# Kernel optimization log

Hardware: AMD Instinct MI355X
Metric: run time of the kernel (lower is better)

The kernel has to match this reference:

```python
import jax, jax.numpy as jnp
import numpy as np

B, T, C = 4, 2048, 1024
N_HEAD = 16
HEAD = C // N_HEAD

def setup_inputs() -> dict:
    key = jax.random.key(0)
    k1, k2, k3 = jax.random.split(key, 3)
    x = jax.random.normal(k1, (B, T, C), dtype=jnp.float32)
    w_attn = jax.random.normal(k2, (C, 3 * C), dtype=jnp.float32) * (1.0 / np.sqrt(C))
    w_proj = jax.random.normal(k3, (C, C), dtype=jnp.float32) * (1.0 / np.sqrt(C))
    return {"x": x, "w_attn": w_attn, "w_proj": w_proj}

def reference(x, w_attn, w_proj):
    b, t, c = x.shape
    qkv = x @ w_attn  # [B,T,3C]
    q, k, v = jnp.split(qkv, 3, axis=-1)
    # [B,T,C] -> [B,H,T,D]
    def heads(z):
        return z.reshape(b, t, N_HEAD, HEAD).transpose(0, 2, 1, 3)
    q, k, v = heads(q), heads(k), heads(v)
    scale = 1.0 / np.sqrt(HEAD)
    att = jnp.einsum('bhqd,bhkd->bhqk', q, k) * scale  # [B,H,T,T]
    causal = jnp.tril(jnp.ones((t, t), dtype=bool))
    att = jnp.where(causal[None, None], att, -jnp.inf)
    att = jax.nn.softmax(att, axis=-1)
    y = jnp.einsum('bhqk,bhkd->bhqd', att, v)  # [B,H,T,D]
    y = y.transpose(0, 2, 1, 3).reshape(b, t, c)
    return y @ w_proj
```

## Files before the change

kernel.cpp:

```cpp
#include <hip/hip_runtime.h>
#include <hip/hip_bf16.h>


typedef __attribute__((ext_vector_type(8))) short bf16x8;
typedef __attribute__((ext_vector_type(4))) float f32x4;
typedef __attribute__((ext_vector_type(16))) float f32x16;

#define T_DIM 2048
#define NHEAD 16
#define HDIM  64

__device__ __forceinline__ unsigned short f2bf(float f) {
    union { float f; unsigned int u; } v; v.f = f;
    unsigned int r = v.u + 0x7fffu + ((v.u >> 16) & 1u);
    return (unsigned short)(r >> 16);
}

__device__ __forceinline__ unsigned cvtpk_bf16(float lo, float hi) {
    unsigned r;
    asm("v_cvt_pk_bf16_f32 %0, %1, %2" : "=v"(r) : "v"(lo), "v"(hi));
    return r;
}
__device__ __forceinline__ void pl32swap(unsigned &x, unsigned &y) {
    asm("v_permlane32_swap_b32 %0, %1" : "+v"(x), "+v"(y));
}
__device__ __forceinline__ bf16x8 mk8(unsigned w0, unsigned w1, unsigned w2, unsigned w3) {
    union { unsigned u[4]; bf16x8 v; } p;
    p.u[0] = w0; p.u[1] = w1; p.u[2] = w2; p.u[3] = w3;
    return p.v;
}

__device__ __forceinline__ void gload_lds16(const void* g, void* l) {
    __builtin_amdgcn_global_load_lds(
        (const __attribute__((address_space(1))) void*)g,
        (__attribute__((address_space(3))) void*)l,
        16, 0, 0);
}

__global__ void cvt_bf16_k(const float* __restrict__ src, unsigned short* __restrict__ dst, int n) {
    int i = (blockIdx.x * blockDim.x + threadIdx.x) * 4;
    if (i < n) {
        float4 v = *(const float4*)(src + i);
        ushort4 o; o.x = f2bf(v.x); o.y = f2bf(v.y); o.z = f2bf(v.z); o.w = f2bf(v.w);
        *(ushort4*)(dst + i) = o;
    }
}

__global__ void transpose_wb_k(const float* __restrict__ src, unsigned short* __restrict__ dst,
                               int R, int Cc) {
    __shared__ float tile[32][33];
    int c0 = blockIdx.x * 32, r0 = blockIdx.y * 32;
    int tx = threadIdx.x & 31, ty = threadIdx.x >> 5;
    #pragma unroll
    for (int i = 0; i < 32; i += 8)
        tile[ty + i][tx] = src[(size_t)(r0 + ty + i) * Cc + c0 + tx];
    __syncthreads();
    #pragma unroll
    for (int i = 0; i < 32; i += 8)
        dst[(size_t)(c0 + ty + i) * R + r0 + tx] = f2bf(tile[tx][ty + i]);
}

template<int EPI>
__global__ __launch_bounds__(512, 2) void gemm_bt_k(
    const unsigned short* __restrict__ A, const unsigned short* __restrict__ Bt,
    void* __restrict__ out0, void* __restrict__ out1, void* __restrict__ out2,
    int M, int N, int K)
{
    extern __shared__ __align__(16) unsigned short smem[];
    unsigned short* sA = smem;
    unsigned short* sB = smem + 49152;

    const int tid = threadIdx.x, lane = tid & 63, wave = tid >> 6;
    const int wm = wave >> 1, wn = wave & 1;
    const int lrow = lane & 15, hi = lane >> 4;

    const int nwg = gridDim.x * gridDim.y;
    const int lin = blockIdx.y * gridDim.x + blockIdx.x;
    const int lin2 = (lin & 7) * (nwg >> 3) + (lin >> 3);
    const int bxg = lin2 % gridDim.x, byg = lin2 / gridDim.x;
    const int row0 = byg * 256, col0 = bxg * 128;

    const int arow = tid >> 3;
    const int gk = ((tid & 7) ^ (arow & 7)) * 8;
    const unsigned short* gA0 = A + (size_t)(row0 + arow) * K + gk;
    const unsigned short* gA1 = A + (size_t)(row0 + arow + 64) * K + gk;
    const unsigned short* gA2 = A + (size_t)(row0 + arow + 128) * K + gk;
    const unsigned short* gA3 = A + (size_t)(row0 + arow + 192) * K + gk;
    const unsigned short* gB0 = Bt + (size_t)(col0 + arow) * K + gk;
    const unsigned short* gB1 = Bt + (size_t)(col0 + arow + 64) * K + gk;

    const int NT = K >> 6;

#define STAGE_P0(ts, sl) { const size_t ko_ = (size_t)(ts) * 64; \
        unsigned short* dA_ = sA + (sl) * 16384; \
        gload_lds16(gA0 + ko_, dA_ + tid * 8); \
        gload_lds16(gA1 + ko_, dA_ + (tid + 512) * 8); \
        gload_lds16(gA2 + ko_, dA_ + (tid + 1024) * 8); }
#define STAGE_P1(ts, sl) { const size_t ko_ = (size_t)(ts) * 64; \
        unsigned short* dA_ = sA + (sl) * 16384; \
        unsigned short* dB_ = sB + (sl) * 8192; \
        gload_lds16(gA3 + ko_, dA_ + (tid + 1536) * 8); \
        gload_lds16(gB0 + ko_, dB_ + tid * 8); \
        gload_lds16(gB1 + ko_, dB_ + (tid + 512) * 8); }

    f32x4 acc[4][4] = {};

    STAGE_P0(0, 0); STAGE_P1(0, 0);
    STAGE_P0(1, 1); STAGE_P1(1, 1);
    asm volatile("s_waitcnt vmcnt(6)" ::: "memory");
    __builtin_amdgcn_s_barrier();
    __builtin_amdgcn_sched_barrier(0);

    int slot = 0;
    for (int t = 0; t < NT; ++t) {
        const int s2 = (slot + 2 >= 3) ? slot - 1 : slot + 2;
        const unsigned short* As = sA + slot * 16384;
        const unsigned short* Bs = sB + slot * 8192;
        bf16x8 af[4], bf_[4];

        {
            const int kc = hi ^ (lrow & 7);
            #pragma unroll
            for (int mi = 0; mi < 4; ++mi)
                af[mi] = *(const bf16x8*)&As[((wm * 64 + mi * 16 + lrow) * 8 + kc) * 8];
            #pragma unroll
            for (int ni = 0; ni < 4; ++ni)
                bf_[ni] = *(const bf16x8*)&Bs[((wn * 64 + ni * 16 + lrow) * 8 + kc) * 8];
        }
        if (t + 2 < NT) STAGE_P0(t + 2, s2);
        __builtin_amdgcn_s_barrier();
        asm volatile("s_waitcnt lgkmcnt(0)" ::: "memory");
        __builtin_amdgcn_sched_barrier(0);
        __builtin_amdgcn_s_setprio(1);
        #pragma unroll
        for (int mi = 0; mi < 4; ++mi)
            #pragma unroll
            for (int ni = 0; ni < 4; ++ni)
                acc[mi][ni] = __builtin_amdgcn_mfma_f32_16x16x32_bf16(af[mi], bf_[ni], acc[mi][ni], 0, 0, 0);
        __builtin_amdgcn_s_setprio(0);
        __builtin_amdgcn_s_barrier();

        {
            const int kc = (4 + hi) ^ (lrow & 7);
            #pragma unroll
            for (int mi = 0; mi < 4; ++mi)
                af[mi] = *(const bf16x8*)&As[((wm * 64 + mi * 16 + lrow) * 8 + kc) * 8];
            #pragma unroll
            for (int ni = 0; ni < 4; ++ni)
                bf_[ni] = *(const bf16x8*)&Bs[((wn * 64 + ni * 16 + lrow) * 8 + kc) * 8];
        }
        if (t + 2 < NT) STAGE_P1(t + 2, s2);
        __builtin_amdgcn_s_barrier();
        asm volatile("s_waitcnt lgkmcnt(0)" ::: "memory");
        __builtin_amdgcn_sched_barrier(0);
        __builtin_amdgcn_s_setprio(1);
        #pragma unroll
        for (int mi = 0; mi < 4; ++mi)
            #pragma unroll
            for (int ni = 0; ni < 4; ++ni)
                acc[mi][ni] = __builtin_amdgcn_mfma_f32_16x16x32_bf16(af[mi], bf_[ni], acc[mi][ni], 0, 0, 0);
        __builtin_amdgcn_s_setprio(0);
        if (t + 2 < NT) { asm volatile("s_waitcnt vmcnt(6)" ::: "memory"); }
        else           { asm volatile("s_waitcnt vmcnt(0)" ::: "memory"); }
        __builtin_amdgcn_s_barrier();
        __builtin_amdgcn_sched_barrier(0);
        slot = (slot + 1 >= 3) ? 0 : slot + 1;
    }
#undef STAGE_P0
#undef STAGE_P1

    if (EPI == 1) {
        #pragma unroll
        for (int mi = 0; mi < 4; ++mi)
            #pragma unroll
            for (int ni = 0; ni < 4; ++ni) {
                int gm0 = row0 + wm * 64 + mi * 16 + hi * 4;
                int gn  = col0 + wn * 64 + ni * 16 + lrow;
                #pragma unroll
                for (int r = 0; r < 4; ++r)
                    ((float*)out0)[(size_t)(gm0 + r) * N + gn] = acc[mi][ni][r];
            }
    } else if (col0 < 1024) {
        const int bb = row0 >> 11;
        #pragma unroll
        for (int mi = 0; mi < 4; ++mi)
            #pragma unroll
            for (int ni = 0; ni < 4; ++ni) {
                int gm0 = row0 + wm * 64 + mi * 16 + hi * 4;
                int gn  = col0 + wn * 64 + ni * 16 + lrow;
                int h = (gn >> 6) & 15, d = gn & 63;
                #pragma unroll
                for (int r = 0; r < 4; ++r) {
                    int t = (gm0 + r) & 2047;
                    ((unsigned short*)out0)[((size_t)(bb * NHEAD + h) * T_DIM + t) * HDIM + d] =
                        f2bf(acc[mi][ni][r] * 0.18033688011112042f);
                }
            }
    } else {
        const bool isK = (col0 < 2048);
        unsigned short* st = smem;
        __syncthreads();
        #pragma unroll
        for (int mi = 0; mi < 4; ++mi) {
            #pragma unroll
            for (int ni = 0; ni < 4; ++ni) {
                const int gnl = wn * 64 + ni * 16 + lrow;
                const int hl = gnl >> 6, d = gnl & 63;
                #pragma unroll
                for (int r = 0; r < 4; ++r) {
                    const int tl = wm * 64 + mi * 16 + hi * 4 + r;
                    int idx;
                    if (isK) idx = (hl * 4 + (tl >> 6)) * 4096 + ((d >> 3) * 64 + (tl & 63)) * 8 + (d & 7);
                    else     idx = (hl * 4 + (tl >> 6)) * 4096 + (((tl >> 3) & 7) * 64 + d) * 8 + (tl & 7);
                    st[idx] = f2bf(acc[mi][ni][r]);
                }
            }
        }
        __syncthreads();
        unsigned short* outb = (unsigned short*)(isK ? out1 : out2);
        const int bb = row0 >> 11;
        const int h0 = (col0 & 1023) >> 6;
        const int tc0 = (row0 & 2047) >> 6;
        #pragma unroll
        for (int seg = 0; seg < 8; ++seg) {
            const int hl = seg >> 2, tc = seg & 3;
            const size_t gbase = ((size_t)(bb * NHEAD + h0 + hl) * 32 + tc0 + tc) * 4096;
            *(uint4*)(outb + gbase + tid * 8) = *(const uint4*)(st + seg * 4096 + tid * 8);
        }
    }
}

__global__ __launch_bounds__(512) void attn_k(
    const unsigned short* __restrict__ qb, const unsigned short* __restrict__ kcm,
    const unsigned short* __restrict__ vcm, unsigned short* __restrict__ yb)
{
    __shared__ __align__(16) unsigned short Ks[2][4096];
    __shared__ __align__(16) unsigned short Vs[2][4096];

    const int tid = threadIdx.x, lane = tid & 63, wave = tid >> 6;
    const int bh = blockIdx.y;
    const int q32 = lane & 31, hi32 = lane >> 5;
    const unsigned short* Kg = kcm + (size_t)bh * 32 * 4096;
    const unsigned short* Vg = vcm + (size_t)bh * 32 * 4096;

    #pragma unroll
    for (int pass = 0; pass < 2; ++pass) {
        const int bxx = (pass == 0) ? (int)blockIdx.x : (7 - (int)blockIdx.x);
        const int ntiles = 4 * bxx + 4;
        const int q0w = bxx * 256 + wave * 32;
        const int qg = q0w + q32;

        const unsigned short* qrow = qb + ((size_t)bh * T_DIM + q0w + q32) * HDIM;
        bf16x8 qf[4];
        #pragma unroll
        for (int kc = 0; kc < 4; ++kc)
            qf[kc] = *(const bf16x8*)(qrow + kc * 16 + hi32 * 8);

        f32x16 o0 = {}, o1 = {};
        float lsum = 0.f;

        gload_lds16(Kg + tid * 8, &Ks[0][tid * 8]);
        gload_lds16(Vg + tid * 8, &Vs[0][tid * 8]);
        __syncthreads();

        int cur = 0;
        for (int jt = 0; jt < ntiles; ++jt) {
            if (jt + 1 < ntiles) {
                gload_lds16(Kg + (size_t)(jt + 1) * 4096 + tid * 8, &Ks[cur ^ 1][tid * 8]);
                gload_lds16(Vg + (size_t)(jt + 1) * 4096 + tid * 8, &Vs[cur ^ 1][tid * 8]);
            }
            if (jt * 64 <= q0w + 31) {
                f32x16 s0 = {}, s1 = {};
                #pragma unroll
                for (int kc = 0; kc < 4; ++kc) {
                    bf16x8 a0 = *(const bf16x8*)&Ks[cur][((kc * 2 + hi32) * 64 + q32) * 8];
                    bf16x8 a1 = *(const bf16x8*)&Ks[cur][((kc * 2 + hi32) * 64 + 32 + q32) * 8];
                    s0 = __builtin_amdgcn_mfma_f32_32x32x16_bf16(a0, qf[kc], s0, 0, 0, 0);
                    s1 = __builtin_amdgcn_mfma_f32_32x32x16_bf16(a1, qf[kc], s1, 0, 0, 0);
                }
                if (jt * 64 + 63 > q0w) {
                    #pragma unroll
                    for (int r = 0; r < 16; ++r) {
                        int kv0 = jt * 64 + (r & 3) + 8 * (r >> 2) + 4 * hi32;
                        if (kv0 > qg)      s0[r] = -1e30f;
                        if (kv0 + 32 > qg) s1[r] = -1e30f;
                    }
                }
                bf16x8 pa[4];
                #pragma unroll
                for (int blk = 0; blk < 2; ++blk) {
                    float p_[16]; unsigned w_[8];
                    #pragma unroll
                    for (int i = 0; i < 16; ++i) {
                        float sv = blk ? s1[i] : s0[i];
                        p_[i] = __builtin_amdgcn_exp2f(sv - 16.0f);
                        lsum += p_[i];
                    }
                    #pragma unroll
                    for (int i = 0; i < 8; ++i) w_[i] = cvtpk_bf16(p_[2 * i], p_[2 * i + 1]);
                    pl32swap(w_[0], w_[2]); pl32swap(w_[1], w_[3]);
                    pl32swap(w_[4], w_[6]); pl32swap(w_[5], w_[7]);
                    pa[blk * 2]     = mk8(w_[0], w_[1], w_[2], w_[3]);
                    pa[blk * 2 + 1] = mk8(w_[4], w_[5], w_[6], w_[7]);
                }
                #pragma unroll
                for (int kvc = 0; kvc < 4; ++kvc) {
                    bf16x8 b0 = *(const bf16x8*)&Vs[cur][((kvc * 2 + hi32) * 64 + q32) * 8];
                    bf16x8 b1 = *(const bf16x8*)&Vs[cur][((kvc * 2 + hi32) * 64 + 32 + q32) * 8];
                    o0 = __builtin_amdgcn_mfma_f32_32x32x16_bf16(pa[kvc], b0, o0, 0, 0, 0);
                    o1 = __builtin_amdgcn_mfma_f32_32x32x16_bf16(pa[kvc], b1, o1, 0, 0, 0);
                }
            }
            __syncthreads();
            cur ^= 1;
        }

        {
            unsigned la = __float_as_uint(lsum), lb = __float_as_uint(lsum);
            pl32swap(la, lb);
            lsum = __uint_as_float(la) + __uint_as_float(lb);
        }
        const int bb2 = bh >> 4, h = bh & 15;
        #pragma unroll
        for (int r = 0; r < 16; ++r) {
            const int cr = (r & 3) + 8 * (r >> 2) + 4 * hi32;
            float inv = 1.0f / __shfl(lsum, cr);
            int t = q0w + cr;
            size_t off = ((size_t)(bb2 * T_DIM + t)) * 1024 + h * HDIM + q32;
            yb[off]      = f2bf(o0[r] * inv);
            yb[off + 32] = f2bf(o1[r] * inv);
        }
    }
}

extern "C" void kernel_launch(void* const* d_in, const int* in_sizes, int n_in,
                              void* d_out, int out_size, void* d_ws, size_t ws_size,
                              hipStream_t stream) {
    const float* x      = (const float*)d_in[0];
    const float* w_attn = (const float*)d_in[1];
    const float* w_proj = (const float*)d_in[2];
    float* out = (float*)d_out;

    unsigned short* xb  = (unsigned short*)d_ws;
    unsigned short* wat = xb  + (size_t)8192 * 1024;
    unsigned short* wpt = wat + (size_t)3072 * 1024;
    unsigned short* qb  = wpt + (size_t)1024 * 1024;
    unsigned short* kcm = qb  + (size_t)64 * 2048 * 64;
    unsigned short* vcm = kcm + (size_t)64 * 2048 * 64;
    unsigned short* yb  = vcm + (size_t)64 * 2048 * 64;

    (void)hipFuncSetAttribute((const void*)gemm_bt_k<0>,
                              hipFuncAttributeMaxDynamicSharedMemorySize, 147456);
    (void)hipFuncSetAttribute((const void*)gemm_bt_k<1>,
                              hipFuncAttributeMaxDynamicSharedMemorySize, 147456);

    cvt_bf16_k<<<8192, 256, 0, stream>>>(x, xb, 8192 * 1024);
    transpose_wb_k<<<dim3(96, 32), 256, 0, stream>>>(w_attn, wat, 1024, 3072);
    transpose_wb_k<<<dim3(32, 32), 256, 0, stream>>>(w_proj, wpt, 1024, 1024);

    gemm_bt_k<0><<<dim3(24, 32), 512, 147456, stream>>>(xb, wat, qb, kcm, vcm, 8192, 3072, 1024);
    attn_k<<<dim3(4, 64), 512, 0, stream>>>(qb, kcm, vcm, yb);
    gemm_bt_k<1><<<dim3(8, 32), 512, 147456, stream>>>(yb, wpt, out, nullptr, nullptr, 8192, 1024, 1024);
}
```

Measured before the change: 167.5 us.

## Enlarge GEMM block tile to 256x256 with 4-stage K32 LDS pipeline

Reworks the bf16 GEMM kernel from a 256x128 tile with a 3-slot, K=64 pipeline to a 256x256 tile split across a 2x4 wave grid. It uses a 4-slot ring of K=32 stages prefetched three steps ahead. Each wave now covers 128x64 outputs, which raises operand reuse per LDS load and halves the number of blocks. The epilogues are adjusted for 8 M sub-tiles and 16 store segments. The trade-off is fewer blocks (384 for QKV, 128 for the output projection), which risks idle CUs and worse wave quantization, plus higher accumulator register pressure.

```diff
diff --git a/kernel.cpp b/kernel.cpp
--- a/kernel.cpp
+++ b/kernel.cpp
@@ -68,66 +68,58 @@
 {
     extern __shared__ __align__(16) unsigned short smem[];
     unsigned short* sA = smem;
-    unsigned short* sB = smem + 49152;
+    unsigned short* sB = smem + 32768;
 
     const int tid = threadIdx.x, lane = tid & 63, wave = tid >> 6;
-    const int wm = wave >> 1, wn = wave & 1;
+    const int wm = wave >> 2, wn = wave & 3;
     const int lrow = lane & 15, hi = lane >> 4;
 
     const int nwg = gridDim.x * gridDim.y;
     const int lin = blockIdx.y * gridDim.x + blockIdx.x;
     const int lin2 = (lin & 7) * (nwg >> 3) + (lin >> 3);
     const int bxg = lin2 % gridDim.x, byg = lin2 / gridDim.x;
-    const int row0 = byg * 256, col0 = bxg * 128;
-
-    const int arow = tid >> 3;
-    const int gk = ((tid & 7) ^ (arow & 7)) * 8;
-    const unsigned short* gA0 = A + (size_t)(row0 + arow) * K + gk;
-    const unsigned short* gA1 = A + (size_t)(row0 + arow + 64) * K + gk;
-    const unsigned short* gA2 = A + (size_t)(row0 + arow + 128) * K + gk;
-    const unsigned short* gA3 = A + (size_t)(row0 + arow + 192) * K + gk;
-    const unsigned short* gB0 = Bt + (size_t)(col0 + arow) * K + gk;
-    const unsigned short* gB1 = Bt + (size_t)(col0 + arow + 64) * K + gk;
-
-    const int NT = K >> 6;
-
-#define STAGE_P0(ts, sl) { const size_t ko_ = (size_t)(ts) * 64; \
-        unsigned short* dA_ = sA + (sl) * 16384; \
-        gload_lds16(gA0 + ko_, dA_ + tid * 8); \
-        gload_lds16(gA1 + ko_, dA_ + (tid + 512) * 8); \
-        gload_lds16(gA2 + ko_, dA_ + (tid + 1024) * 8); }
-#define STAGE_P1(ts, sl) { const size_t ko_ = (size_t)(ts) * 64; \
-        unsigned short* dA_ = sA + (sl) * 16384; \
-        unsigned short* dB_ = sB + (sl) * 8192; \
-        gload_lds16(gA3 + ko_, dA_ + (tid + 1536) * 8); \
-        gload_lds16(gB0 + ko_, dB_ + tid * 8); \
-        gload_lds16(gB1 + ko_, dB_ + (tid + 512) * 8); }
-
-    f32x4 acc[4][4] = {};
-
-    STAGE_P0(0, 0); STAGE_P1(0, 0);
-    STAGE_P0(1, 1); STAGE_P1(1, 1);
-    asm volatile("s_waitcnt vmcnt(6)" ::: "memory");
+    const int row0 = byg * 256, col0 = bxg * 256;
+
+    const int arow = tid >> 2;
+    const int gkw = ((tid & 3) ^ (arow & 3)) * 8;
+    const unsigned short* gA0 = A + (size_t)(row0 + arow) * K + gkw;
+    const unsigned short* gA1 = A + (size_t)(row0 + arow + 128) * K + gkw;
+    const unsigned short* gB0 = Bt + (size_t)(col0 + arow) * K + gkw;
+    const unsigned short* gB1 = Bt + (size_t)(col0 + arow + 128) * K + gkw;
+
+    const int NU = K >> 5;
+
+#define STAGE_A(u) { const size_t ko_ = (size_t)(u) * 32; \
+        unsigned short* d_ = sA + ((u) & 3) * 8192; \
+        gload_lds16(gA0 + ko_, d_ + tid * 8); \
+        gload_lds16(gA1 + ko_, d_ + (tid + 512) * 8); }
+#define STAGE_B(u) { const size_t ko_ = (size_t)(u) * 32; \
+        unsigned short* d_ = sB + ((u) & 3) * 8192; \
+        gload_lds16(gB0 + ko_, d_ + tid * 8); \
+        gload_lds16(gB1 + ko_, d_ + (tid + 512) * 8); }
+
+    f32x4 acc[8][4] = {};
+
+    STAGE_A(0); STAGE_B(0);
+    STAGE_A(1); STAGE_B(1);
+    STAGE_A(2); STAGE_B(2);
+    asm volatile("s_waitcnt vmcnt(8)" ::: "memory");
     __builtin_amdgcn_s_barrier();
     __builtin_amdgcn_sched_barrier(0);
 
-    int slot = 0;
-    for (int t = 0; t < NT; ++t) {
-        const int s2 = (slot + 2 >= 3) ? slot - 1 : slot + 2;
-        const unsigned short* As = sA + slot * 16384;
-        const unsigned short* Bs = sB + slot * 8192;
-        bf16x8 af[4], bf_[4];
-
-        {
-            const int kc = hi ^ (lrow & 7);
-            #pragma unroll
-            for (int mi = 0; mi < 4; ++mi)
-                af[mi] = *(const bf16x8*)&As[((wm * 64 + mi * 16 + lrow) * 8 + kc) * 8];
-            #pragma unroll
-            for (int ni = 0; ni < 4; ++ni)
-                bf_[ni] = *(const bf16x8*)&Bs[((wn * 64 + ni * 16 + lrow) * 8 + kc) * 8];
-        }
-        if (t + 2 < NT) STAGE_P0(t + 2, s2);
+    const int kc = hi ^ (lrow & 3);
+    for (int u = 0; u < NU; ++u) {
+        const unsigned short* As = sA + (u & 3) * 8192;
+        const unsigned short* Bs = sB + (u & 3) * 8192;
+        bf16x8 bfr[4], afr[4];
+
+        #pragma unroll
+        for (int ni = 0; ni < 4; ++ni)
+            bfr[ni] = *(const bf16x8*)&Bs[((wn * 64 + ni * 16 + lrow) * 4 + kc) * 8];
+        #pragma unroll
+        for (int mi = 0; mi < 4; ++mi)
+            afr[mi] = *(const bf16x8*)&As[((wm * 128 + mi * 16 + lrow) * 4 + kc) * 8];
+        if (u + 3 < NU) STAGE_A(u + 3);
         __builtin_amdgcn_s_barrier();
         asm volatile("s_waitcnt lgkmcnt(0)" ::: "memory");
         __builtin_amdgcn_sched_barrier(0);
@@ -136,20 +128,14 @@
         for (int mi = 0; mi < 4; ++mi)
             #pragma unroll
             for (int ni = 0; ni < 4; ++ni)
-                acc[mi][ni] = __builtin_amdgcn_mfma_f32_16x16x32_bf16(af[mi], bf_[ni], acc[mi][ni], 0, 0, 0);
+                acc[mi][ni] = __builtin_amdgcn_mfma_f32_16x16x32_bf16(afr[mi], bfr[ni], acc[mi][ni], 0, 0, 0);
         __builtin_amdgcn_s_setprio(0);
         __builtin_amdgcn_s_barrier();
 
-        {
-            const int kc = (4 + hi) ^ (lrow & 7);
-            #pragma unroll
-            for (int mi = 0; mi < 4; ++mi)
-                af[mi] = *(const bf16x8*)&As[((wm * 64 + mi * 16 + lrow) * 8 + kc) * 8];
-            #pragma unroll
-            for (int ni = 0; ni < 4; ++ni)
-                bf_[ni] = *(const bf16x8*)&Bs[((wn * 64 + ni * 16 + lrow) * 8 + kc) * 8];
-        }
-        if (t + 2 < NT) STAGE_P1(t + 2, s2);
+        #pragma unroll
+        for (int mi = 0; mi < 4; ++mi)
+            afr[mi] = *(const bf16x8*)&As[((wm * 128 + (mi + 4) * 16 + lrow) * 4 + kc) * 8];
+        if (u + 3 < NU) STAGE_B(u + 3);
         __builtin_amdgcn_s_barrier();
         asm volatile("s_waitcnt lgkmcnt(0)" ::: "memory");
         __builtin_amdgcn_sched_barrier(0);
@@ -158,23 +144,23 @@
         for (int mi = 0; mi < 4; ++mi)
             #pragma unroll
             for (int ni = 0; ni < 4; ++ni)
-                acc[mi][ni] = __builtin_amdgcn_mfma_f32_16x16x32_bf16(af[mi], bf_[ni], acc[mi][ni], 0, 0, 0);
+                acc[mi + 4][ni] = __builtin_amdgcn_mfma_f32_16x16x32_bf16(afr[mi], bfr[ni], acc[mi + 4][ni], 0, 0, 0);
         __builtin_amdgcn_s_setprio(0);
-        if (t + 2 < NT) { asm volatile("s_waitcnt vmcnt(6)" ::: "memory"); }
-        else           { asm volatile("s_waitcnt vmcnt(0)" ::: "memory"); }
+        if (u + 3 < NU)      { asm volatile("s_waitcnt vmcnt(8)" ::: "memory"); }
+        else if (u + 2 < NU) { asm volatile("s_waitcnt vmcnt(4)" ::: "memory"); }
+        else                 { asm volatile("s_waitcnt vmcnt(0)" ::: "memory"); }
         __builtin_amdgcn_s_barrier();
         __builtin_amdgcn_sched_barrier(0);
-        slot = (slot + 1 >= 3) ? 0 : slot + 1;
     }
-#undef STAGE_P0
-#undef STAGE_P1
+#undef STAGE_A
+#undef STAGE_B
 
     if (EPI == 1) {
         #pragma unroll
-        for (int mi = 0; mi < 4; ++mi)
+        for (int mi = 0; mi < 8; ++mi)
             #pragma unroll
             for (int ni = 0; ni < 4; ++ni) {
-                int gm0 = row0 + wm * 64 + mi * 16 + hi * 4;
+                int gm0 = row0 + wm * 128 + mi * 16 + hi * 4;
                 int gn  = col0 + wn * 64 + ni * 16 + lrow;
                 #pragma unroll
                 for (int r = 0; r < 4; ++r)
@@ -183,10 +169,10 @@
     } else if (col0 < 1024) {
         const int bb = row0 >> 11;
         #pragma unroll
-        for (int mi = 0; mi < 4; ++mi)
+        for (int mi = 0; mi < 8; ++mi)
             #pragma unroll
             for (int ni = 0; ni < 4; ++ni) {
-                int gm0 = row0 + wm * 64 + mi * 16 + hi * 4;
+                int gm0 = row0 + wm * 128 + mi * 16 + hi * 4;
                 int gn  = col0 + wn * 64 + ni * 16 + lrow;
                 int h = (gn >> 6) & 15, d = gn & 63;
                 #pragma unroll
@@ -201,14 +187,14 @@
         unsigned short* st = smem;
         __syncthreads();
         #pragma unroll
-        for (int mi = 0; mi < 4; ++mi) {
+        for (int mi = 0; mi < 8; ++mi) {
             #pragma unroll
             for (int ni = 0; ni < 4; ++ni) {
                 const int gnl = wn * 64 + ni * 16 + lrow;
                 const int hl = gnl >> 6, d = gnl & 63;
                 #pragma unroll
                 for (int r = 0; r < 4; ++r) {
-                    const int tl = wm * 64 + mi * 16 + hi * 4 + r;
+                    const int tl = wm * 128 + mi * 16 + hi * 4 + r;
                     int idx;
                     if (isK) idx = (hl * 4 + (tl >> 6)) * 4096 + ((d >> 3) * 64 + (tl & 63)) * 8 + (d & 7);
                     else     idx = (hl * 4 + (tl >> 6)) * 4096 + (((tl >> 3) & 7) * 64 + d) * 8 + (tl & 7);
@@ -219,10 +205,10 @@
         __syncthreads();
         unsigned short* outb = (unsigned short*)(isK ? out1 : out2);
         const int bb = row0 >> 11;
-        const int h0 = (col0 & 1023) >> 6;
+        const int h0 = ((col0 - 1024) & 1023) >> 6;
         const int tc0 = (row0 & 2047) >> 6;
         #pragma unroll
-        for (int seg = 0; seg < 8; ++seg) {
+        for (int seg = 0; seg < 16; ++seg) {
             const int hl = seg >> 2, tc = seg & 3;
             const size_t gbase = ((size_t)(bb * NHEAD + h0 + hl) * 32 + tc0 + tc) * 4096;
             *(uint4*)(outb + gbase + tid * 8) = *(const uint4*)(st + seg * 4096 + tid * 8);
@@ -350,15 +336,15 @@
     unsigned short* yb  = vcm + (size_t)64 * 2048 * 64;
 
     (void)hipFuncSetAttribute((const void*)gemm_bt_k<0>,
-                              hipFuncAttributeMaxDynamicSharedMemorySize, 147456);
+                              hipFuncAttributeMaxDynamicSharedMemorySize, 131072);
     (void)hipFuncSetAttribute((const void*)gemm_bt_k<1>,
-                              hipFuncAttributeMaxDynamicSharedMemorySize, 147456);
+                              hipFuncAttributeMaxDynamicSharedMemorySize, 131072);
 
     cvt_bf16_k<<<8192, 256, 0, stream>>>(x, xb, 8192 * 1024);
     transpose_wb_k<<<dim3(96, 32), 256, 0, stream>>>(w_attn, wat, 1024, 3072);
     transpose_wb_k<<<dim3(32, 32), 256, 0, stream>>>(w_proj, wpt, 1024, 1024);
 
-    gemm_bt_k<0><<<dim3(24, 32), 512, 147456, stream>>>(xb, wat, qb, kcm, vcm, 8192, 3072, 1024);
+    gemm_bt_k<0><<<dim3(12, 32), 512, 131072, stream>>>(xb, wat, qb, kcm, vcm, 8192, 3072, 1024);
     attn_k<<<dim3(4, 64), 512, 0, stream>>>(qb, kcm, vcm, yb);
-    gemm_bt_k<1><<<dim3(8, 32), 512, 147456, stream>>>(yb, wpt, out, nullptr, nullptr, 8192, 1024, 1024);
-}
+    gemm_bt_k<1><<<dim3(4, 32), 512, 131072, stream>>>(yb, wpt, out, nullptr, nullptr, 8192, 1024, 1024);
+}
```

Result: slower. 188.2 us (+12.4%).
